# Kernel tuning notes

Measured on AMD Instinct MI355X. Metric: run time of the kernel, lower is better.

The kernel has to match this reference:

```python
import jax, jax.numpy as jnp
import numpy as np

B, N, M, F, BF = 16, 1024, 12, 64, 128
N_CONV = 3
VOCAB = 100
BN_EPS = 1e-3  # keras BatchNormalization default epsilon


def _bn(x, gamma, beta):
    # inference-mode BN with moving_mean=0, moving_var=1 (keras defaults)
    return gamma * (x * (1.0 / jnp.sqrt(1.0 + BN_EPS))) + beta


def setup_inputs() -> dict:
    key = jax.random.key(0)
    ks = jax.random.split(key, 16)
    in_fea = 2 * F + BF
    inp = {
        'atom_types': jax.random.randint(ks[0], (B, N), 0, VOCAB, dtype=jnp.int32),
        'bond_fea': jax.random.normal(ks[1], (B, N, M, BF), dtype=jnp.float32),
        'nbr_list': jax.random.randint(ks[2], (B, N, M), 0, N, dtype=jnp.int32),
        'target_index': jax.random.randint(ks[3], (B, 64), 0, N, dtype=jnp.int32),
        'emb': jax.random.normal(ks[4], (VOCAB, F), dtype=jnp.float32) * 0.05,
        'core_w': jax.random.normal(ks[5], (N_CONV, in_fea, F), dtype=jnp.float32) / np.sqrt(in_fea),
        'core_b': jnp.zeros((N_CONV, F), dtype=jnp.float32),
        'filt_w': jax.random.normal(ks[6], (N_CONV, in_fea, 1), dtype=jnp.float32) / np.sqrt(in_fea),
        'filt_b': jnp.zeros((N_CONV, 1), dtype=jnp.float32),
        'bna_g': jnp.ones((N_CONV, F), dtype=jnp.float32),
        'bna_b': jnp.zeros((N_CONV, F), dtype=jnp.float32),
        'bnb_g': jnp.ones((N_CONV, F), dtype=jnp.float32),
        'bnb_b': jnp.zeros((N_CONV, F), dtype=jnp.float32),
        'dense_w': jax.random.normal(ks[7], (F, F), dtype=jnp.float32) / np.sqrt(F),
        'dense_b': jnp.zeros((F,), dtype=jnp.float32),
    }
    return inp


def _cgcnn_layer(x, bond_fea, nbr_list, cw, cb, fw, fb, bag, bab, bbg, bbb):
    # x: (B,N,F); bond_fea: (B,N,M,BF); nbr_list: (B,N,M)
    bidx = jnp.arange(x.shape[0])[:, None, None]
    atom_nbr = x[bidx, nbr_list]                       # (B,N,M,F) gather_nd
    atom_self = jnp.broadcast_to(x[:, :, None, :], atom_nbr.shape)
    total = jnp.concatenate([atom_self, atom_nbr, bond_fea], axis=-1)  # (B,N,M,2F+BF)
    core = total @ cw + cb                             # (B,N,M,F)
    filt = total @ fw + fb                             # (B,N,M,1)
    core = _bn(core, bag, bab)
    filt = jax.nn.softmax(filt, axis=2)                # softmax over neighbors
    core = jax.nn.relu(core)
    summed = jnp.mean(filt * core, axis=2)             # (B,N,F)
    summed = _bn(summed, bbg, bbb)
    return jax.nn.relu(x + summed)


def reference(atom_types, bond_fea, nbr_list, target_index, emb, core_w, core_b,
              filt_w, filt_b, bna_g, bna_b, bnb_g, bnb_b, dense_w, dense_b):
    x = emb[atom_types]                                # (B,N,F)
    for l in range(N_CONV):
        x = _cgcnn_layer(x, bond_fea, nbr_list, core_w[l], core_b[l],
                         filt_w[l], filt_b[l], bna_g[l], bna_b[l], bnb_g[l], bnb_b[l])
    bidx = jnp.arange(x.shape[0])[:, None]
    crys = x[bidx, target_index]                       # (B,N0,F) pooling gather
    crys = jax.nn.relu(crys)
    out = jax.nn.relu(crys @ dense_w + dense_b)        # (B,N0,F)
    return out
```

## Files before the change

### kernel.cpp

```cpp
#include <hip/hip_runtime.h>
#include <hip/hip_bf16.h>


#define BB 16
#define NN 1024
#define MM 12
#define FF 64
#define BFE 128
#define RT (BB * NN * MM)
#define S_BN 0.99950037f
#define WCOLS 208
#define WSTR 136

typedef __attribute__((ext_vector_type(8))) short bf16x8;
typedef __attribute__((ext_vector_type(4))) float f32x4;

static __device__ __forceinline__ unsigned short f2bf(float f) {
    union { float f; unsigned u; } c; c.f = f;
    unsigned r = c.u + 0x7fff + ((c.u >> 16) & 1);
    return (unsigned short)(r >> 16);
}
static __device__ __forceinline__ float bf2f(unsigned short s) {
    union { unsigned u; float f; } c; c.u = ((unsigned)s) << 16;
    return c.f;
}

__global__ void fold_w(const float* __restrict__ cw, const float* __restrict__ cb,
                       const float* __restrict__ g,  const float* __restrict__ bab,
                       float* __restrict__ cwp, float* __restrict__ cbp) {
    int i = blockIdx.x * 256 + threadIdx.x;
    if (i >= 3 * 256 * 64) return;
    int f = i & 63;
    int l = i / (256 * 64);
    float gs = g[l * 64 + f] * S_BN;
    cwp[i] = cw[i] * gs;
    if (((i >> 6) & 255) == 0)
        cbp[l * 64 + f] = cb[l * 64 + f] * gs + bab[l * 64 + f];
}

__global__ void prep_wT(const float* __restrict__ cw, const float* __restrict__ g,
                        const float* __restrict__ fw, unsigned short* __restrict__ wT) {
    int i = blockIdx.x * 256 + threadIdx.x;
    if (i >= WCOLS * WSTR) return;
    int col = i / WSTR, k = i % WSTR;
    float v = 0.f;
    if (k < 128) {
        if (col < 192) {
            int l = col >> 6, f = col & 63;
            v = cw[(l * 256 + 128 + k) * 64 + f] * g[l * 64 + f] * S_BN;
        } else if (col < 195) {
            int l = col - 192;
            v = fw[l * 256 + 128 + k];
        }
    }
    wT[i] = f2bf(v);
}

__global__ void embed_k(const int* __restrict__ at, const float* __restrict__ emb,
                        float* __restrict__ x) {
    int i = blockIdx.x * 256 + threadIdx.x;
    int f = i & 63;
    int bn = i >> 6;
    x[i] = emb[at[bn] * FF + f];
}

__global__ __launch_bounds__(256) void gemm_bond(
    const float* __restrict__ bond, const unsigned short* __restrict__ wT,
    unsigned short* __restrict__ core, float* __restrict__ filt) {
    __shared__ unsigned short bsh[WCOLS * WSTR];
    __shared__ unsigned short ash[64 * WSTR];
    int tid = threadIdx.x;
    int w = tid >> 6, lane = tid & 63;
    int row0 = blockIdx.x * 64;

    const float4* wsrc = (const float4*)wT;
    float4* wdst = (float4*)bsh;
    #pragma unroll
    for (int i = 0; i < 14; i++) {
        int idx = tid + 256 * i;
        if (idx < (WCOLS * WSTR * 2) / 16) wdst[idx] = wsrc[idx];
    }
    const float4* bsrc = (const float4*)(bond + (size_t)row0 * BFE);
    #pragma unroll
    for (int i = 0; i < 8; i++) {
        int idx = tid + 256 * i;
        float4 v = bsrc[idx];
        int r = idx >> 5, c4 = idx & 31;
        ushort4 h;
        h.x = f2bf(v.x); h.y = f2bf(v.y); h.z = f2bf(v.z); h.w = f2bf(v.w);
        *(ushort4*)&ash[r * WSTR + c4 * 4] = h;
    }
    __syncthreads();

    int m = lane & 15, quad = lane >> 4;
    f32x4 acc[13];
    #pragma unroll
    for (int t = 0; t < 13; t++) acc[t] = (f32x4){0.f, 0.f, 0.f, 0.f};

    #pragma unroll
    for (int c = 0; c < 4; c++) {
        bf16x8 af = *(const bf16x8*)&ash[(w * 16 + m) * WSTR + c * 32 + quad * 8];
        #pragma unroll
        for (int t = 0; t < 13; t++) {
            bf16x8 bfv = *(const bf16x8*)&bsh[(t * 16 + m) * WSTR + c * 32 + quad * 8];
            acc[t] = __builtin_amdgcn_mfma_f32_16x16x32_bf16(af, bfv, acc[t], 0, 0, 0);
        }
    }

    int rbase = row0 + w * 16 + quad * 4;
    #pragma unroll
    for (int t = 0; t < 12; t++) {
        int l = t >> 2;
        int f = (t & 3) * 16 + m;
        #pragma unroll
        for (int r = 0; r < 4; r++)
            core[((size_t)l * RT + rbase + r) * 64 + f] = f2bf(acc[t][r]);
    }
    if (m < 3) {
        #pragma unroll
        for (int r = 0; r < 4; r++)
            filt[(size_t)m * RT + rbase + r] = acc[12][r];
    }
}

__global__ __launch_bounds__(256) void atomproj(
    const float* __restrict__ x, const float* __restrict__ cwp_l,
    const float* __restrict__ cbp_l, const float* __restrict__ fw_l,
    const float* __restrict__ fb_l,
    float* __restrict__ ys, float* __restrict__ yn,
    float* __restrict__ fs, float* __restrict__ fn) {
    __shared__ float wsh[128 * 64];
    __shared__ float xs[4][64];
    int tid = threadIdx.x, w = tid >> 6, lane = tid & 63;
    #pragma unroll
    for (int i = 0; i < 8; i++)
        ((float4*)wsh)[tid + 256 * i] = ((const float4*)cwp_l)[tid + 256 * i];
    float fw1 = fw_l[lane], fw2 = fw_l[64 + lane];
    float cb = cbp_l[lane], fbv = fb_l[0];
    __syncthreads();
    #pragma unroll 1
    for (int it = 0; it < 4; it++) {
        int row = (blockIdx.x * 4 + it) * 4 + w;
        float xl = x[(size_t)row * 64 + lane];
        xs[w][lane] = xl;
        float a1 = cb, a2 = 0.f;
        #pragma unroll 16
        for (int k = 0; k < 64; k++) {
            float xv = xs[w][k];
            a1 += xv * wsh[k * 64 + lane];
            a2 += xv * wsh[(64 + k) * 64 + lane];
        }
        ys[(size_t)row * 64 + lane] = a1;
        yn[(size_t)row * 64 + lane] = a2;
        float p1 = xl * fw1, p2 = xl * fw2;
        #pragma unroll
        for (int off = 32; off; off >>= 1) {
            p1 += __shfl_xor(p1, off, 64);
            p2 += __shfl_xor(p2, off, 64);
        }
        if (lane == 0) { fs[row] = p1 + fbv; fn[row] = p2; }
    }
}

__global__ __launch_bounds__(256) void layer_ep(
    const float* __restrict__ x, const unsigned short* __restrict__ core_l,
    const float* __restrict__ filt_l, const int* __restrict__ nbr,
    const float* __restrict__ ys, const float* __restrict__ yn,
    const float* __restrict__ fs, const float* __restrict__ fn,
    const float* __restrict__ bbg, const float* __restrict__ bbb,
    float* __restrict__ xout) {
    int tid = threadIdx.x, w = tid >> 6, lane = tid & 63;
    int row = blockIdx.x * 4 + w;
    int base = (row >> 10) * NN;
    size_t rb = (size_t)row * MM;

    int jv[MM]; float fltv[MM], corev[MM];
    #pragma unroll
    for (int mm = 0; mm < MM; mm++) jv[mm] = nbr[rb + mm];
    float fsv = fs[row], ysv = ys[(size_t)row * 64 + lane];
    #pragma unroll
    for (int mm = 0; mm < MM; mm++)
        fltv[mm] = filt_l[rb + mm] + fsv + fn[base + jv[mm]];
    #pragma unroll
    for (int mm = 0; mm < MM; mm++)
        corev[mm] = bf2f(core_l[(rb + mm) * 64 + lane]) + ysv
                  + yn[(size_t)(base + jv[mm]) * 64 + lane];
    float fmax = -1e30f;
    #pragma unroll
    for (int mm = 0; mm < MM; mm++) fmax = fmaxf(fmax, fltv[mm]);
    float fsum = 0.f;
    #pragma unroll
    for (int mm = 0; mm < MM; mm++) { fltv[mm] = __expf(fltv[mm] - fmax); fsum += fltv[mm]; }
    float inv = 1.f / (12.f * fsum);
    float summed = 0.f;
    #pragma unroll
    for (int mm = 0; mm < MM; mm++) summed += fltv[mm] * fmaxf(corev[mm], 0.f);
    summed *= inv;
    float o = x[(size_t)row * 64 + lane] + bbg[lane] * (summed * S_BN) + bbb[lane];
    xout[(size_t)row * 64 + lane] = fmaxf(o, 0.f);
}

__global__ __launch_bounds__(256) void final_k(
    const float* __restrict__ x, const int* __restrict__ tidx,
    const float* __restrict__ dw, const float* __restrict__ db,
    float* __restrict__ out) {
    __shared__ float xs[4][64];
    __shared__ float wsh[64 * 64];
    int tid = threadIdx.x;
    int w = tid >> 6, lane = tid & 63;
    const float4* src = (const float4*)dw;
    float4* dst = (float4*)wsh;
    #pragma unroll
    for (int i = 0; i < 4; i++) dst[tid + 256 * i] = src[tid + 256 * i];
    int row = blockIdx.x * 4 + w;
    int b = row >> 6;
    int t = tidx[row];
    float xv = x[((size_t)b * NN + t) * 64 + lane];
    xs[w][lane] = fmaxf(xv, 0.f);
    __syncthreads();
    float a = db[lane];
    #pragma unroll 16
    for (int k = 0; k < 64; k++) a += xs[w][k] * wsh[k * 64 + lane];
    out[row * 64 + lane] = fmaxf(a, 0.f);
}

extern "C" void kernel_launch(void* const* d_in, const int* in_sizes, int n_in,
                              void* d_out, int out_size, void* d_ws, size_t ws_size,
                              hipStream_t stream) {
    const int*   at   = (const int*)d_in[0];
    const float* bond = (const float*)d_in[1];
    const int*   nbr  = (const int*)d_in[2];
    const int*   tgt  = (const int*)d_in[3];
    const float* emb  = (const float*)d_in[4];
    const float* cw   = (const float*)d_in[5];
    const float* cb   = (const float*)d_in[6];
    const float* fw   = (const float*)d_in[7];
    const float* fb   = (const float*)d_in[8];
    const float* bag  = (const float*)d_in[9];
    const float* bab  = (const float*)d_in[10];
    const float* bbg  = (const float*)d_in[11];
    const float* bbb  = (const float*)d_in[12];
    const float* dw   = (const float*)d_in[13];
    const float* db   = (const float*)d_in[14];

    float* ws   = (float*)d_ws;
    float* xA   = ws;
    float* xB   = xA + (size_t)BB * NN * FF;
    float* cwp  = xB + (size_t)BB * NN * FF;
    float* cbp  = cwp + 3 * 256 * 64;
    float* ys   = cbp + 192;
    float* yn   = ys + (size_t)BB * NN * FF;
    float* fs   = yn + (size_t)BB * NN * FF;
    float* fn   = fs + (size_t)BB * NN;
    float* filt = fn + (size_t)BB * NN;
    unsigned short* wT   = (unsigned short*)(filt + 3 * (size_t)RT);
    unsigned short* core = wT + WCOLS * WSTR;

    fold_w<<<(3 * 256 * 64 + 255) / 256, 256, 0, stream>>>(cw, cb, bag, bab, cwp, cbp);
    prep_wT<<<(WCOLS * WSTR + 255) / 256, 256, 0, stream>>>(cw, bag, fw, wT);
    embed_k<<<(BB * NN * FF) / 256, 256, 0, stream>>>(at, emb, xA);
    gemm_bond<<<RT / 64, 256, 0, stream>>>(bond, wT, core, filt);

    float* xin = xA;
    float* xout = xB;
    for (int l = 0; l < 3; l++) {
        atomproj<<<BB * NN / 16, 256, 0, stream>>>(
            xin, cwp + (size_t)l * 256 * 64, cbp + l * 64, fw + l * 256, fb + l,
            ys, yn, fs, fn);
        layer_ep<<<BB * NN / 4, 256, 0, stream>>>(
            xin, core + (size_t)l * RT * 64, filt + (size_t)l * RT, nbr,
            ys, yn, fs, fn, bbg + l * 64, bbb + l * 64, xout);
        float* t = xin; xin = xout; xout = t;
    }

    final_k<<<BB * 64 / 4, 256, 0, stream>>>(xin, tgt, dw, db, (float*)d_out);
}
```

Before: 290.1 us.

## Fuse bond GEMM into per-layer conv epilogue, dropping core/filt intermediates

Removes the standalone bond-feature GEMM and its bf16 core/filter intermediate buffers, computing each layer's bond projection inside the conv epilogue kernel with weights held in registers and results staged in LDS. This eliminates writing and re-reading the large per-edge intermediates and one kernel launch. In exchange, the fp32 bond tensor is re-read and re-projected once per layer instead of once total, and the grid becomes small (512 blocks) with each wave loading strided rows.

```diff
diff --git a/kernel.cpp b/kernel.cpp
--- a/kernel.cpp
+++ b/kernel.cpp
@@ -6,11 +6,8 @@
 #define NN 1024
 #define MM 12
 #define FF 64
-#define BFE 128
-#define RT (BB * NN * MM)
 #define S_BN 0.99950037f
-#define WCOLS 208
-#define WSTR 136
+#define CSTR 74
 
 typedef __attribute__((ext_vector_type(8))) short bf16x8;
 typedef __attribute__((ext_vector_type(4))) float f32x4;
@@ -38,22 +35,22 @@
         cbp[l * 64 + f] = cb[l * 64 + f] * gs + bab[l * 64 + f];
 }
 
-__global__ void prep_wT(const float* __restrict__ cw, const float* __restrict__ g,
-                        const float* __restrict__ fw, unsigned short* __restrict__ wT) {
+__global__ void prep_wT2(const float* __restrict__ cw, const float* __restrict__ g,
+                         const float* __restrict__ fw, unsigned short* __restrict__ wT2) {
     int i = blockIdx.x * 256 + threadIdx.x;
-    if (i >= WCOLS * WSTR) return;
-    int col = i / WSTR, k = i % WSTR;
+    if (i >= 30720) return;
+    int j = i & 7;
+    int t = i >> 3;
+    int lane = t & 63;  t >>= 6;
+    int ct = t % 5;     t /= 5;
+    int kc = t & 3;
+    int l  = t >> 2;
+    int col = ct * 16 + (lane & 15);
+    int k   = kc * 32 + (lane >> 4) * 8 + j;
     float v = 0.f;
-    if (k < 128) {
-        if (col < 192) {
-            int l = col >> 6, f = col & 63;
-            v = cw[(l * 256 + 128 + k) * 64 + f] * g[l * 64 + f] * S_BN;
-        } else if (col < 195) {
-            int l = col - 192;
-            v = fw[l * 256 + 128 + k];
-        }
-    }
-    wT[i] = f2bf(v);
+    if (col < 64)       v = cw[(l * 256 + 128 + k) * 64 + col] * g[l * 64 + col] * S_BN;
+    else if (col == 64) v = fw[l * 256 + 128 + k];
+    wT2[i] = f2bf(v);
 }
 
 __global__ void embed_k(const int* __restrict__ at, const float* __restrict__ emb,
@@ -62,65 +59,6 @@
     int f = i & 63;
     int bn = i >> 6;
     x[i] = emb[at[bn] * FF + f];
-}
-
-__global__ __launch_bounds__(256) void gemm_bond(
-    const float* __restrict__ bond, const unsigned short* __restrict__ wT,
-    unsigned short* __restrict__ core, float* __restrict__ filt) {
-    __shared__ unsigned short bsh[WCOLS * WSTR];
-    __shared__ unsigned short ash[64 * WSTR];
-    int tid = threadIdx.x;
-    int w = tid >> 6, lane = tid & 63;
-    int row0 = blockIdx.x * 64;
-
-    const float4* wsrc = (const float4*)wT;
-    float4* wdst = (float4*)bsh;
-    #pragma unroll
-    for (int i = 0; i < 14; i++) {
-        int idx = tid + 256 * i;
-        if (idx < (WCOLS * WSTR * 2) / 16) wdst[idx] = wsrc[idx];
-    }
-    const float4* bsrc = (const float4*)(bond + (size_t)row0 * BFE);
-    #pragma unroll
-    for (int i = 0; i < 8; i++) {
-        int idx = tid + 256 * i;
-        float4 v = bsrc[idx];
-        int r = idx >> 5, c4 = idx & 31;
-        ushort4 h;
-        h.x = f2bf(v.x); h.y = f2bf(v.y); h.z = f2bf(v.z); h.w = f2bf(v.w);
-        *(ushort4*)&ash[r * WSTR + c4 * 4] = h;
-    }
-    __syncthreads();
-
-    int m = lane & 15, quad = lane >> 4;
-    f32x4 acc[13];
-    #pragma unroll
-    for (int t = 0; t < 13; t++) acc[t] = (f32x4){0.f, 0.f, 0.f, 0.f};
-
-    #pragma unroll
-    for (int c = 0; c < 4; c++) {
-        bf16x8 af = *(const bf16x8*)&ash[(w * 16 + m) * WSTR + c * 32 + quad * 8];
-        #pragma unroll
-        for (int t = 0; t < 13; t++) {
-            bf16x8 bfv = *(const bf16x8*)&bsh[(t * 16 + m) * WSTR + c * 32 + quad * 8];
-            acc[t] = __builtin_amdgcn_mfma_f32_16x16x32_bf16(af, bfv, acc[t], 0, 0, 0);
-        }
-    }
-
-    int rbase = row0 + w * 16 + quad * 4;
-    #pragma unroll
-    for (int t = 0; t < 12; t++) {
-        int l = t >> 2;
-        int f = (t & 3) * 16 + m;
-        #pragma unroll
-        for (int r = 0; r < 4; r++)
-            core[((size_t)l * RT + rbase + r) * 64 + f] = f2bf(acc[t][r]);
-    }
-    if (m < 3) {
-        #pragma unroll
-        for (int r = 0; r < 4; r++)
-            filt[(size_t)m * RT + rbase + r] = acc[12][r];
-    }
 }
 
 __global__ __launch_bounds__(256) void atomproj(
@@ -162,42 +100,109 @@
     }
 }
 
-__global__ __launch_bounds__(256) void layer_ep(
-    const float* __restrict__ x, const unsigned short* __restrict__ core_l,
-    const float* __restrict__ filt_l, const int* __restrict__ nbr,
+__global__ __launch_bounds__(256, 2) void conv_fused(
+    const float* __restrict__ bond, const unsigned short* __restrict__ wTl,
+    const int* __restrict__ nbr, const float* __restrict__ x,
     const float* __restrict__ ys, const float* __restrict__ yn,
     const float* __restrict__ fs, const float* __restrict__ fn,
     const float* __restrict__ bbg, const float* __restrict__ bbb,
     float* __restrict__ xout) {
+    __shared__ unsigned short csh[4][48 * CSTR];
+    __shared__ float fltw[4][48];
     int tid = threadIdx.x, w = tid >> 6, lane = tid & 63;
-    int row = blockIdx.x * 4 + w;
-    int base = (row >> 10) * NN;
-    size_t rb = (size_t)row * MM;
-
-    int jv[MM]; float fltv[MM], corev[MM];
+    int mcol = lane & 15, q = lane >> 4;
+
+    bf16x8 bw[4][5];
     #pragma unroll
-    for (int mm = 0; mm < MM; mm++) jv[mm] = nbr[rb + mm];
-    float fsv = fs[row], ysv = ys[(size_t)row * 64 + lane];
-    #pragma unroll
-    for (int mm = 0; mm < MM; mm++)
-        fltv[mm] = filt_l[rb + mm] + fsv + fn[base + jv[mm]];
-    #pragma unroll
-    for (int mm = 0; mm < MM; mm++)
-        corev[mm] = bf2f(core_l[(rb + mm) * 64 + lane]) + ysv
-                  + yn[(size_t)(base + jv[mm]) * 64 + lane];
-    float fmax = -1e30f;
-    #pragma unroll
-    for (int mm = 0; mm < MM; mm++) fmax = fmaxf(fmax, fltv[mm]);
-    float fsum = 0.f;
-    #pragma unroll
-    for (int mm = 0; mm < MM; mm++) { fltv[mm] = __expf(fltv[mm] - fmax); fsum += fltv[mm]; }
-    float inv = 1.f / (12.f * fsum);
-    float summed = 0.f;
-    #pragma unroll
-    for (int mm = 0; mm < MM; mm++) summed += fltv[mm] * fmaxf(corev[mm], 0.f);
-    summed *= inv;
-    float o = x[(size_t)row * 64 + lane] + bbg[lane] * (summed * S_BN) + bbb[lane];
-    xout[(size_t)row * 64 + lane] = fmaxf(o, 0.f);
+    for (int kc = 0; kc < 4; kc++)
+        #pragma unroll
+        for (int ct = 0; ct < 5; ct++)
+            bw[kc][ct] = *(const bf16x8*)(wTl + ((kc * 5 + ct) * 64 + lane) * 8);
+
+    #pragma unroll 1
+    for (int t = 0; t < 2; t++) {
+        int tile = blockIdx.x * 2 + t;
+        int rowbase = tile * 192 + w * 48;
+
+        f32x4 acc[3][5];
+        #pragma unroll
+        for (int rt = 0; rt < 3; rt++)
+            #pragma unroll
+            for (int ct = 0; ct < 5; ct++)
+                acc[rt][ct] = (f32x4){0.f, 0.f, 0.f, 0.f};
+
+        #pragma unroll
+        for (int kc = 0; kc < 4; kc++) {
+            #pragma unroll
+            for (int rt = 0; rt < 3; rt++) {
+                const float* ap = bond + (size_t)(rowbase + rt * 16 + mcol) * 128
+                                + kc * 32 + q * 8;
+                float4 v0 = *(const float4*)ap;
+                float4 v1 = *(const float4*)(ap + 4);
+                bf16x8 af;
+                af[0] = (short)f2bf(v0.x); af[1] = (short)f2bf(v0.y);
+                af[2] = (short)f2bf(v0.z); af[3] = (short)f2bf(v0.w);
+                af[4] = (short)f2bf(v1.x); af[5] = (short)f2bf(v1.y);
+                af[6] = (short)f2bf(v1.z); af[7] = (short)f2bf(v1.w);
+                #pragma unroll
+                for (int ct = 0; ct < 5; ct++)
+                    acc[rt][ct] = __builtin_amdgcn_mfma_f32_16x16x32_bf16(
+                        af, bw[kc][ct], acc[rt][ct], 0, 0, 0);
+            }
+        }
+
+        #pragma unroll
+        for (int rt = 0; rt < 3; rt++)
+            #pragma unroll
+            for (int r = 0; r < 4; r++) {
+                int row = rt * 16 + q * 4 + r;
+                #pragma unroll
+                for (int ct = 0; ct < 4; ct++)
+                    csh[w][row * CSTR + ct * 16 + mcol] = f2bf(acc[rt][ct][r]);
+                if (mcol == 0) fltw[w][row] = acc[rt][4][r];
+            }
+        __syncthreads();
+
+        int atom = tile * 16 + w * 4 + q;
+        int base = (atom >> 10) << 10;
+        int jv[MM]; float lg[MM];
+        #pragma unroll
+        for (int m = 0; m < MM; m++) jv[m] = nbr[atom * MM + m];
+        float fsv = fs[atom];
+        #pragma unroll
+        for (int m = 0; m < MM; m++)
+            lg[m] = fltw[w][q * MM + m] + fsv + fn[base + jv[m]];
+        float mx = -1e30f;
+        #pragma unroll
+        for (int m = 0; m < MM; m++) mx = fmaxf(mx, lg[m]);
+        float sme = 0.f;
+        #pragma unroll
+        for (int m = 0; m < MM; m++) { lg[m] = __expf(lg[m] - mx); sme += lg[m]; }
+        float inv = 1.f / (12.f * sme);
+
+        float ysv[4], sum[4] = {0.f, 0.f, 0.f, 0.f};
+        #pragma unroll
+        for (int ct = 0; ct < 4; ct++)
+            ysv[ct] = ys[(size_t)atom * 64 + ct * 16 + mcol];
+        #pragma unroll
+        for (int m = 0; m < MM; m++) {
+            const float* ynr = yn + (size_t)(base + jv[m]) * 64;
+            int row = q * MM + m;
+            #pragma unroll
+            for (int ct = 0; ct < 4; ct++) {
+                float c = bf2f(csh[w][row * CSTR + ct * 16 + mcol])
+                        + ysv[ct] + ynr[ct * 16 + mcol];
+                sum[ct] += lg[m] * fmaxf(c, 0.f);
+            }
+        }
+        #pragma unroll
+        for (int ct = 0; ct < 4; ct++) {
+            int f = ct * 16 + mcol;
+            float o = x[(size_t)atom * 64 + f] + bbg[f] * (sum[ct] * inv * S_BN) + bbb[f];
+            xout[(size_t)atom * 64 + f] = fmaxf(o, 0.f);
+        }
+        __syncthreads();
+    }
 }
 
 __global__ __launch_bounds__(256) void final_k(
@@ -243,23 +248,20 @@
     const float* dw   = (const float*)d_in[13];
     const float* db   = (const float*)d_in[14];
 
-    float* ws   = (float*)d_ws;
-    float* xA   = ws;
-    float* xB   = xA + (size_t)BB * NN * FF;
-    float* cwp  = xB + (size_t)BB * NN * FF;
-    float* cbp  = cwp + 3 * 256 * 64;
-    float* ys   = cbp + 192;
-    float* yn   = ys + (size_t)BB * NN * FF;
-    float* fs   = yn + (size_t)BB * NN * FF;
-    float* fn   = fs + (size_t)BB * NN;
-    float* filt = fn + (size_t)BB * NN;
-    unsigned short* wT   = (unsigned short*)(filt + 3 * (size_t)RT);
-    unsigned short* core = wT + WCOLS * WSTR;
+    float* ws  = (float*)d_ws;
+    float* xA  = ws;
+    float* xB  = xA + (size_t)BB * NN * FF;
+    float* cwp = xB + (size_t)BB * NN * FF;
+    float* cbp = cwp + 3 * 256 * 64;
+    float* ys  = cbp + 192;
+    float* yn  = ys + (size_t)BB * NN * FF;
+    float* fs  = yn + (size_t)BB * NN * FF;
+    float* fn  = fs + (size_t)BB * NN;
+    unsigned short* wT2 = (unsigned short*)(fn + (size_t)BB * NN);
 
     fold_w<<<(3 * 256 * 64 + 255) / 256, 256, 0, stream>>>(cw, cb, bag, bab, cwp, cbp);
-    prep_wT<<<(WCOLS * WSTR + 255) / 256, 256, 0, stream>>>(cw, bag, fw, wT);
+    prep_wT2<<<120, 256, 0, stream>>>(cw, bag, fw, wT2);
     embed_k<<<(BB * NN * FF) / 256, 256, 0, stream>>>(at, emb, xA);
-    gemm_bond<<<RT / 64, 256, 0, stream>>>(bond, wT, core, filt);
 
     float* xin = xA;
     float* xout = xB;
@@ -267,8 +269,8 @@
         atomproj<<<BB * NN / 16, 256, 0, stream>>>(
             xin, cwp + (size_t)l * 256 * 64, cbp + l * 64, fw + l * 256, fb + l,
             ys, yn, fs, fn);
-        layer_ep<<<BB * NN / 4, 256, 0, stream>>>(
-            xin, core + (size_t)l * RT * 64, filt + (size_t)l * RT, nbr,
+        conv_fused<<<512, 256, 0, stream>>>(
+            bond, wT2 + (size_t)l * 10240, nbr, xin,
             ys, yn, fs, fn, bbg + l * 64, bbb + l * 64, xout);
         float* t = xin; xin = xout; xout = t;
     }
```

After: 300.9 us. 3.7% more time.
